# Performance work log

Measured on AMD Instinct MI355X. Metric: run time of the kernel, lower is better.

The kernel has to match this reference:

```python
import jax, jax.numpy as jnp
import numpy as np

N = 100000        # n_nodes (entities)
B = 1024          # batch of users
S = 32            # edge_threshold (sampled edges per node)
M = 64            # adj_matrix neighbors per node
D_IN = 64         # in_channel[0]
HID = 32          # out_channel[0] == in_channel[1]
D_OUT = 64        # out_channel[1]
K_STEP = 2
NUM_SAMPLE = 32
ITEM_LO, ITEM_HI = 0, 39999
SLOPE = 0.01      # leaky_relu default negative slope


def setup_inputs() -> dict:
    key = jax.random.key(0)
    ks = jax.random.split(key, 12)
    sc = lambda *sh: 1.0 / np.sqrt(sh[-1])
    return {
        "entity_embedding": jax.random.normal(ks[0], (N, D_IN), jnp.float32) * 0.1,
        "W1l": jax.random.normal(ks[1], (HID, D_IN), jnp.float32) * sc(HID, D_IN),
        "W1r": jax.random.normal(ks[2], (HID, D_IN), jnp.float32) * sc(HID, D_IN),
        "b1": jnp.zeros((HID,), jnp.float32),
        "W2l": jax.random.normal(ks[3], (D_OUT, HID), jnp.float32) * sc(D_OUT, HID),
        "W2r": jax.random.normal(ks[4], (D_OUT, HID), jnp.float32) * sc(D_OUT, HID),
        "b2": jnp.zeros((D_OUT,), jnp.float32),
        "disc_emb": jax.random.normal(ks[5], (N, D_OUT), jnp.float32) * 0.1,
        "users": jax.random.randint(ks[6], (B,), 0, ITEM_HI + 1, jnp.int32),
        "pos": jax.random.randint(ks[7], (B,), 0, ITEM_HI + 1, jnp.int32),
        "adj_matrix": jax.random.randint(ks[8], (N, M), 0, N, jnp.int32),
        "edge_matrix": jax.random.randint(ks[9], (N, S), 0, N, jnp.int32),
    }


def _leaky(x):
    return jnp.where(x >= 0, x, SLOPE * x)


def _sage(x, src, dst, Wl, Wr, b):
    # PyG SAGEConv: lin_l(mean_{j->i} x_j) + lin_r(x_i)
    sums = jax.ops.segment_sum(x[src], dst, num_segments=N)
    cnt = jax.ops.segment_sum(jnp.ones(src.shape, x.dtype), dst, num_segments=N)
    mean = sums / jnp.maximum(cnt, 1.0)[:, None]
    return mean @ Wl.T + b + x @ Wr.T


def _gcn(x, src, dst, W1l, W1r, b1, W2l, W2r, b2):
    h = _leaky(_sage(x, src, dst, W1l, W1r, b1))   # dropout = identity (eval)
    h = _sage(h, src, dst, W2l, W2r, b2)
    nrm = jnp.sqrt(jnp.sum(h * h, axis=1, keepdims=True))
    return h / jnp.maximum(nrm, 1e-12)             # F.normalize


def _kg_step(gcn, pos_idx, users, adj, explore_flag, step):
    u_e = gcn[users]                               # [B, d]
    pos_e = gcn[pos_idx]                           # [B, d]
    one_hop = adj[pos_idx] if explore_flag == 1 else adj[users]   # [B, M]
    i_e = gcn[one_hop]                             # [B, M, d]
    p = jnp.einsum('bmd,bd->bm', _leaky(pos_e[:, None, :] * i_e), u_e)
    logits = jax.nn.softmax(p, axis=1)
    if step == 1:
        nid = jnp.argmax(logits, axis=1)[:, None]
    else:
        _, nid = jax.lax.top_k(logits, NUM_SAMPLE)
    cand = jnp.take_along_axis(one_hop, nid, axis=1)
    prob = jnp.log(jnp.take_along_axis(logits, nid, axis=1))
    if step == 1:
        return cand[:, 0], prob[:, 0]
    return cand, prob


def _filter_entity(cand, key):
    rnd = jax.random.randint(key, cand.shape, ITEM_LO, ITEM_HI + 1, dtype=cand.dtype)
    bad = (cand > ITEM_HI) | (cand < ITEM_LO)
    return jnp.where(bad, rnd, cand)


def _prune_step(disc_emb, users, pos2, negs, logits):
    # stand-in for discriminator.item_rank (no_grad in original)
    u = jax.lax.stop_gradient(disc_emb[users])
    ranking = jnp.einsum('bd,bjd->bj', u,
                         jax.lax.stop_gradient(disc_emb[pos2] - disc_emb[negs]))
    idx = jnp.argmin(ranking, axis=1)[:, None]
    good_neg = jnp.take_along_axis(negs, idx, axis=1)[:, 0]
    good_logits = jnp.take_along_axis(logits, idx, axis=1)[:, 0]
    return good_neg, good_logits


def reference(entity_embedding, W1l, W1r, b1, W2l, W2r, b2, disc_emb,
              users, pos, adj_matrix, edge_matrix):
    src = jnp.repeat(jnp.arange(N, dtype=jnp.int32), S)   # build_edge node_index
    dst = edge_matrix.reshape(-1)
    gcn = _gcn(entity_embedding, src, dst, W1l, W1r, b1, W2l, W2r, b2)
    fkey = jax.random.key(123)
    neg_list, prob_list = [], []
    p = pos
    for k in range(K_STEP):
        one_hop, one_hop_logits = _kg_step(gcn, p, users, adj_matrix, 1, 1)
        cand, two_logits = _kg_step(gcn, one_hop, users, adj_matrix, 1, 2)
        cand = _filter_entity(cand, jax.random.fold_in(fkey, 2 * k))
        pos2, _ = _kg_step(gcn, p, users, adj_matrix, 2, 2)
        pos2 = _filter_entity(pos2, jax.random.fold_in(fkey, 2 * k + 1))
        good_neg, good_logits = _prune_step(disc_emb, users, pos2, cand, two_logits)
        good_logits = good_logits + one_hop_logits
        neg_list.append(good_neg)
        prob_list.append(good_logits)
        p = good_neg
    return jnp.stack(neg_list), jnp.stack(prob_list)
```

## Files before the change

### kernel.cpp

```cpp
#include <hip/hip_runtime.h>
#include <hip/hip_bf16.h>

#define N_NODES 100000
#define N_EDGES (N_NODES * 32)
#define BATCH   1024
#define SPAN    40000u
#define MULT    7296u
#define FILL_B  (N_EDGES / 256)

#define NB_BKT 391
#define EPB    4096
#define SBLK   782
#define BKT_CAP 8960


__host__ __device__ inline void threefry2x32(unsigned k0, unsigned k1,
                                             unsigned x0, unsigned x1,
                                             unsigned* o0, unsigned* o1)
{
  unsigned ks2 = k0 ^ k1 ^ 0x1BD11BDAu;
  unsigned v0 = x0 + k0, v1 = x1 + k1;
#define RL(x,d) (((x) << (d)) | ((x) >> (32 - (d))))
#define G4(a,b,c,dd) \
  v0 += v1; v1 = RL(v1,a);  v1 ^= v0; \
  v0 += v1; v1 = RL(v1,b);  v1 ^= v0; \
  v0 += v1; v1 = RL(v1,c);  v1 ^= v0; \
  v0 += v1; v1 = RL(v1,dd); v1 ^= v0;
  G4(13,15,26,6)  v0 += k1;  v1 += ks2 + 1u;
  G4(17,29,16,24) v0 += ks2; v1 += k0 + 2u;
  G4(13,15,26,6)  v0 += k0;  v1 += k1 + 3u;
  G4(17,29,16,24) v0 += k1;  v1 += ks2 + 4u;
  G4(13,15,26,6)  v0 += ks2; v1 += k0 + 5u;
#undef G4
#undef RL
  *o0 = v0; *o1 = v1;
}

__device__ __forceinline__ float bcastf(float v, int l)
{
  return __int_as_float(__builtin_amdgcn_readlane(__float_as_int(v), l));
}


__global__ void k_init_buckets(int* __restrict__ bbase, int* __restrict__ bcur)
{
  int i = blockIdx.x * 256 + threadIdx.x;
  if (i < NB_BKT) { bbase[i] = i * BKT_CAP; bcur[i] = i * BKT_CAP; }
}

__global__ __launch_bounds__(256) void k_bucket_hist(
    const int* __restrict__ edge, int* __restrict__ bhist)
{
  __shared__ int h[NB_BKT];
  for (int i = threadIdx.x; i < NB_BKT; i += 256) h[i] = 0;
  __syncthreads();
  int base = blockIdx.x * EPB;
  int cnt = N_EDGES - base; if (cnt > EPB) cnt = EPB;
  const int4* e4 = (const int4*)(edge + base);
  int nq = cnt >> 2;
  for (int i = threadIdx.x; i < nq; i += 256) {
    int4 v = e4[i];
    atomicAdd(&h[v.x >> 8], 1); atomicAdd(&h[v.y >> 8], 1);
    atomicAdd(&h[v.z >> 8], 1); atomicAdd(&h[v.w >> 8], 1);
  }
  __syncthreads();
  for (int i = threadIdx.x; i < NB_BKT; i += 256)
    if (h[i]) atomicAdd(&bhist[i], h[i]);
}

__global__ void k_scan_buckets(const int* __restrict__ bhist,
                               int* __restrict__ bbase, int* __restrict__ bcur)
{
  __shared__ int s[512];
  int t = threadIdx.x;
  s[t] = (t < NB_BKT) ? bhist[t] : 0;
  __syncthreads();
  for (int o = 1; o < 512; o <<= 1) {
    int u = (t >= o) ? s[t - o] : 0;
    __syncthreads();
    s[t] += u;
    __syncthreads();
  }
  if (t < NB_BKT) {
    int excl = s[t] - bhist[t];
    bbase[t] = excl;
    bcur[t]  = excl;
  }
}

__global__ __launch_bounds__(256) void k_bucket_scatter(
    const int* __restrict__ edge, int* __restrict__ bcur,
    int* __restrict__ pairs)
{
  __shared__ int  h[NB_BKT];
  __shared__ int  lbase[NB_BKT];
  __shared__ int  gbase[NB_BKT];
  __shared__ int  lcur[NB_BKT];
  __shared__ int2 buf[EPB];
  int t = threadIdx.x;
  for (int i = t; i < NB_BKT; i += 256) h[i] = 0;
  __syncthreads();
  int base = blockIdx.x * EPB;
  int cnt = N_EDGES - base; if (cnt > EPB) cnt = EPB;
  const int4* e4 = (const int4*)(edge + base);
  int nq = cnt >> 2;
  for (int i = t; i < nq; i += 256) {
    int4 v = e4[i];
    atomicAdd(&h[v.x >> 8], 1); atomicAdd(&h[v.y >> 8], 1);
    atomicAdd(&h[v.z >> 8], 1); atomicAdd(&h[v.w >> 8], 1);
  }
  __syncthreads();
  if (t < 64) {
    int run = 0;
    for (int c = 0; c < NB_BKT; c += 64) {
      int idx = c + t;
      int v = (idx < NB_BKT) ? h[idx] : 0;
      int orig = v;
      for (int o = 1; o < 64; o <<= 1) {
        int u = __shfl_up(v, o);
        if (t >= o) v += u;
      }
      if (idx < NB_BKT) lbase[idx] = run + v - orig;
      run += __shfl(v, 63);
    }
  }
  __syncthreads();
  for (int i = t; i < NB_BKT; i += 256) lcur[i] = lbase[i];
  __syncthreads();
  for (int i = t; i < nq; i += 256) {
    int4 v = e4[i];
    int eid = base + (i << 2);
    int p;
    p = atomicAdd(&lcur[v.x >> 8], 1); buf[p] = make_int2(v.x, (eid + 0) >> 5);
    p = atomicAdd(&lcur[v.y >> 8], 1); buf[p] = make_int2(v.y, (eid + 1) >> 5);
    p = atomicAdd(&lcur[v.z >> 8], 1); buf[p] = make_int2(v.z, (eid + 2) >> 5);
    p = atomicAdd(&lcur[v.w >> 8], 1); buf[p] = make_int2(v.w, (eid + 3) >> 5);
  }
  __syncthreads();
  for (int i = t; i < NB_BKT; i += 256) {
    int c = lcur[i] - lbase[i];
    gbase[i] = (c > 0) ? atomicAdd(&bcur[i], c) : 0;
  }
  __syncthreads();
  for (int i = t; i < cnt; i += 256) {
    int2 pr = buf[i];
    int b = pr.x >> 8;
    pairs[gbase[b] + (i - lbase[b])] = (pr.y << 8) | (pr.x & 255);
  }
}

__global__ __launch_bounds__(256) void k_bucket_csr(
    const int* __restrict__ bbase, const int* __restrict__ bcur,
    const int* __restrict__ pairs, int* __restrict__ csr,
    int* __restrict__ rowp, int* __restrict__ deg)
{
  __shared__ int nd[256], nb[256], nc[256];
  int b = blockIdx.x, t = threadIdx.x;
  int nb0 = b << 8;
  int ebase = bbase[b];
  int ecnt  = bcur[b] - ebase;
  nd[t] = 0; nc[t] = 0;
  __syncthreads();
  for (int i = t; i < ecnt; i += 256) {
    int pr = pairs[ebase + i];
    atomicAdd(&nd[pr & 255], 1);
  }
  __syncthreads();
  nb[t] = nd[t];
  __syncthreads();
  for (int o = 1; o < 256; o <<= 1) {
    int u = (t >= o) ? nb[t - o] : 0;
    __syncthreads();
    nb[t] += u;
    __syncthreads();
  }
  int excl = nb[t] - nd[t];
  int node = nb0 + t;
  if (node < N_NODES) { rowp[node] = ebase + excl; deg[node] = nd[t]; }
  __syncthreads();
  nb[t] = excl;
  __syncthreads();
  for (int i = t; i < ecnt; i += 256) {
    int pr = pairs[ebase + i];
    int l = pr & 255;
    int p = atomicAdd(&nc[l], 1);
    csr[ebase + nb[l] + p] = pr >> 8;
  }
}

__global__ __launch_bounds__(256) void k_gather_csr(
    const int* __restrict__ rowp, const int* __restrict__ deg,
    const int* __restrict__ csr, const float* __restrict__ src,
    float* __restrict__ out)
{
  int node = blockIdx.x * 8 + (threadIdx.x >> 5);
  int f = threadIdx.x & 31;
  int hb = threadIdx.x & 32;
  int sub = f >> 3;
  int q   = f & 7;
  int start = rowp[node];
  int dg = deg[node];
  const float4* src4 = (const float4*)src;
  float4 a0 = make_float4(0.f, 0.f, 0.f, 0.f);
  float4 a1 = make_float4(0.f, 0.f, 0.f, 0.f);
  for (int b0 = 0; b0 < dg; b0 += 32) {
    int idx = b0 + f;
    int e = (idx < dg) ? csr[start + idx] : -1;
#pragma unroll
    for (int j = 0; j < 8; j += 2) {
      int e0 = __shfl(e, hb + 4 * j + sub);
      int e1 = __shfl(e, hb + 4 * (j + 1) + sub);
      if (e0 >= 0) {
        float4 v = src4[(size_t)e0 * 8 + q];
        a0.x += v.x; a0.y += v.y; a0.z += v.z; a0.w += v.w;
      }
      if (e1 >= 0) {
        float4 v = src4[(size_t)e1 * 8 + q];
        a1.x += v.x; a1.y += v.y; a1.z += v.z; a1.w += v.w;
      }
    }
  }
  a0.x += a1.x; a0.y += a1.y; a0.z += a1.z; a0.w += a1.w;
  a0.x += __shfl_xor(a0.x, 8);  a0.y += __shfl_xor(a0.y, 8);
  a0.z += __shfl_xor(a0.z, 8);  a0.w += __shfl_xor(a0.w, 8);
  a0.x += __shfl_xor(a0.x, 16); a0.y += __shfl_xor(a0.y, 16);
  a0.z += __shfl_xor(a0.z, 16); a0.w += __shfl_xor(a0.w, 16);
  if (sub == 0) ((float4*)out)[(size_t)node * 8 + q] = a0;
}

__global__ __launch_bounds__(256) void k_fill_gemm(
    const int* __restrict__ edge, int* __restrict__ head, int* __restrict__ next,
    int nsub, const float* __restrict__ x, const float* __restrict__ W,
    float* __restrict__ y)
{
  __shared__ float sw[32 * 65];
  if (blockIdx.x < FILL_B) {
    int e = blockIdx.x * 256 + threadIdx.x;
    int d = edge[e];
    int sub = e & (nsub - 1);
    int old = atomicExch(head + sub * N_NODES + d, e);
    next[e] = old;
  } else {
    for (int t = threadIdx.x; t < 2048; t += 256) sw[(t >> 6) * 65 + (t & 63)] = W[t];
    __syncthreads();
    int i = (blockIdx.x - FILL_B) * 8 + (threadIdx.x >> 5);
    int f = threadIdx.x & 31;
    const float* xr = x + (size_t)i * 64;
    const float* wr = sw + f * 65;
    float acc = 0.f;
#pragma unroll
    for (int d = 0; d < 64; ++d) acc += xr[d] * wr[d];
    y[(size_t)i * 32 + f] = acc;
  }
}

template<int NSUB>
__global__ __launch_bounds__(256) void k_gather_ll(
    const int* __restrict__ head, const int* __restrict__ next,
    const float* __restrict__ src, float* __restrict__ out,
    int* __restrict__ deg_out)
{
  int node = blockIdx.x * 8 + (threadIdx.x >> 5);
  int f = threadIdx.x & 31;
  int hb = threadIdx.x & 32;
  int e = (f < NSUB) ? head[f * N_NODES + node] : -1;
  float acc = 0.f;
  int cnt = 0;
  while (true) {
    int es[NSUB];
    bool any = false;
#pragma unroll
    for (int j = 0; j < NSUB; ++j) { es[j] = __shfl(e, hb + j); any |= (es[j] != -1); }
    if (!any) break;
    int en = -1;
    if (f < NSUB && e != -1) en = next[e];
#pragma unroll
    for (int j = 0; j < NSUB; ++j)
      if (es[j] != -1) { acc += src[(size_t)(es[j] >> 5) * 32 + f]; cnt++; }
    e = en;
  }
  out[(size_t)node * 32 + f] = acc;
  if (deg_out != nullptr && f == 0) deg_out[node] = cnt;
}

#define DGB 391

__global__ __launch_bounds__(256, 4) void k_gemm64x32(
    const float* __restrict__ x, const float* __restrict__ W, float* __restrict__ y)
{
  int lane = threadIdx.x & 63;
  int wv = blockIdx.x * 4 + (threadIdx.x >> 6);
  int node = wv * 64 + lane;
  bool ok = node < N_NODES;
  const float4* x4 = (const float4*)(x + (size_t)node * 64);
  const float4* W4 = (const float4*)W;
  float acc[32];
#pragma unroll
  for (int o = 0; o < 32; ++o) acc[o] = 0.f;
#pragma unroll 1
  for (int j = 0; j < 16; ++j) {
    float4 xv = ok ? x4[j] : make_float4(0.f, 0.f, 0.f, 0.f);
#pragma unroll
    for (int o = 0; o < 32; ++o) {
      float4 wv4 = W4[o * 16 + j];
      acc[o] += wv4.x * xv.x;
      acc[o] += wv4.y * xv.y;
      acc[o] += wv4.z * xv.z;
      acc[o] += wv4.w * xv.w;
    }
  }
  if (ok) {
    float4* y4 = (float4*)(y + (size_t)node * 32);
#pragma unroll
    for (int k = 0; k < 8; ++k)
      y4[k] = make_float4(acc[4 * k], acc[4 * k + 1], acc[4 * k + 2], acc[4 * k + 3]);
  }
}

__global__ __launch_bounds__(256) void k_scatter(
    const int* __restrict__ edge, const float* __restrict__ src,
    float* __restrict__ acc, int* __restrict__ cnt)
{
  int e = blockIdx.x * 8 + (threadIdx.x >> 5);
  int f = threadIdx.x & 31;
  int d = edge[e];
  atomicAdd(acc + (size_t)d * 32 + f, src[(size_t)(e >> 5) * 32 + f]);
  if (cnt != nullptr && f == 0) atomicAdd(cnt + d, 1);
}

__global__ __launch_bounds__(256, 4) void k_layer1(
    const float* __restrict__ sum1, const int* __restrict__ cnt,
    const float* __restrict__ x, const float* __restrict__ W1r,
    const float* __restrict__ b1, float* __restrict__ h)
{
  int lane = threadIdx.x & 63;
  int wv = blockIdx.x * 4 + (threadIdx.x >> 6);
  int node = wv * 64 + lane;
  bool ok = node < N_NODES;
  const float4* x4 = (const float4*)(x + (size_t)node * 64);
  const float4* W4 = (const float4*)W1r;
  float acc[32];
#pragma unroll
  for (int o = 0; o < 32; ++o) acc[o] = 0.f;
#pragma unroll 1
  for (int j = 0; j < 16; ++j) {
    float4 xv = ok ? x4[j] : make_float4(0.f, 0.f, 0.f, 0.f);
#pragma unroll
    for (int o = 0; o < 32; ++o) {
      float4 wv4 = W4[o * 16 + j];
      acc[o] += wv4.x * xv.x;
      acc[o] += wv4.y * xv.y;
      acc[o] += wv4.z * xv.z;
      acc[o] += wv4.w * xv.w;
    }
  }
  if (ok) {
    float c = fmaxf((float)cnt[node], 1.f);
    const float4* s4 = (const float4*)(sum1 + (size_t)node * 32);
    float4* h4 = (float4*)(h + (size_t)node * 32);
#pragma unroll
    for (int k = 0; k < 8; ++k) {
      float4 sv = s4[k];
      float4 r;
      r.x = ((sv.x / c) + b1[4 * k + 0]) + acc[4 * k + 0];
      r.y = ((sv.y / c) + b1[4 * k + 1]) + acc[4 * k + 1];
      r.z = ((sv.z / c) + b1[4 * k + 2]) + acc[4 * k + 2];
      r.w = ((sv.w / c) + b1[4 * k + 3]) + acc[4 * k + 3];
      r.x = (r.x >= 0.f) ? r.x : 0.01f * r.x;
      r.y = (r.y >= 0.f) ? r.y : 0.01f * r.y;
      r.z = (r.z >= 0.f) ? r.z : 0.01f * r.z;
      r.w = (r.w >= 0.f) ? r.w : 0.01f * r.w;
      h4[k] = r;
    }
  }
}

#define L2_BLOCKS 1250
#define L2_NPW    20
__global__ __launch_bounds__(256) void k_layer2(
    float* __restrict__ A, float* __restrict__ B, const int* __restrict__ cnt,
    const float* __restrict__ W2l, const float* __restrict__ W2r,
    const float* __restrict__ b2)
{
  int lane = threadIdx.x & 63;
  int gw = blockIdx.x * 4 + (threadIdx.x >> 6);
  float wl[32], wr[32];
#pragma unroll
  for (int f = 0; f < 32; ++f) { wl[f] = W2l[lane * 32 + f]; wr[f] = W2r[lane * 32 + f]; }
  float bb = b2[lane];
  int n0 = gw * L2_NPW;
#pragma unroll 1
  for (int i = n0; i < n0 + L2_NPW; ++i) {
    float c = fmaxf((float)cnt[i], 1.f);
    float vin;
    if (lane < 32) vin = B[(size_t)i * 32 + lane] / c;
    else           vin = A[(size_t)i * 32 + (lane - 32)];
    float acc = 0.f, acc2 = 0.f;
#pragma unroll
    for (int f = 0; f < 32; ++f) {
      acc  += bcastf(vin, f)      * wl[f];
      acc2 += bcastf(vin, 32 + f) * wr[f];
    }
    float t = (acc + bb) + acc2;
    float s = t * t;
#pragma unroll
    for (int o = 32; o > 0; o >>= 1) s += __shfl_xor(s, o);
    float g = t / fmaxf(sqrtf(s), 1e-12f);
    if (lane < 32) A[(size_t)i * 32 + lane]        = g;
    else           B[(size_t)i * 32 + (lane - 32)] = g;
  }
}


__device__ inline float kg_score_lds(const float* __restrict__ row,
                                     const float* sp, const float* su)
{
  float acc = 0.f;
#pragma unroll
  for (int d = 0; d < 64; ++d) {
    float t = sp[d] * row[d];
    t = (t >= 0.f) ? t : 0.01f * t;
    acc += t * su[d];
  }
  return acc;
}

__device__ inline float wave_softmax(float acc)
{
  float m = acc;
#pragma unroll
  for (int o = 32; o > 0; o >>= 1) m = fmaxf(m, __shfl_xor(m, o));
  float e = expf(acc - m);
  float Z = e;
#pragma unroll
  for (int o = 32; o > 0; o >>= 1) Z += __shfl_xor(Z, o);
  return e / Z;
}

__device__ inline void load_row(const float* glo, const float* ghi, int node,
                                int lane, float* smem)
{
  smem[lane] = (lane < 32) ? glo[(size_t)node * 32 + lane]
                           : ghi[(size_t)node * 32 + (lane - 32)];
}

__device__ inline void stage_rows(const float* __restrict__ glo,
                                  const float* __restrict__ ghi,
                                  int nb, int lane, float* sn)
{
#pragma unroll
  for (int j = 0; j < 64; ++j) {
    int rj = __builtin_amdgcn_readlane(nb, j);
    float v = (lane < 32) ? glo[(size_t)rj * 32 + lane]
                          : ghi[(size_t)rj * 32 + (lane - 32)];
    sn[j * 65 + lane] = v;
  }
}

__global__ __launch_bounds__(64) void k_kg_argmax(
    const float* __restrict__ glo, const float* __restrict__ ghi,
    const int* __restrict__ users, const int* __restrict__ pvec,
    const int* __restrict__ adj, int* __restrict__ sel_out,
    float* __restrict__ logit_out)
{
  int b = blockIdx.x, lane = threadIdx.x;
  int u = users[b], pb = pvec[b];
  __shared__ float su[64], sp[64];
  __shared__ float sn[64 * 65];
  load_row(glo, ghi, u,  lane, su);
  load_row(glo, ghi, pb, lane, sp);
  int nb = adj[(size_t)pb * 64 + lane];
  stage_rows(glo, ghi, nb, lane, sn);
  __syncthreads();
  float sm = wave_softmax(kg_score_lds(sn + lane * 65, sp, su));
  float v = sm; int i = lane;
#pragma unroll
  for (int o = 32; o > 0; o >>= 1) {
    float ov = __shfl_xor(v, o); int oi = __shfl_xor(i, o);
    if (ov > v || (ov == v && oi < i)) { v = ov; i = oi; }
  }
  float smw = __shfl(sm, i);
  int sel = __shfl(nb, i);
  if (lane == 0) { sel_out[b] = sel; logit_out[b] = logf(smw); }
}

__global__ __launch_bounds__(64) void k_kg_topk2(
    const float* __restrict__ glo, const float* __restrict__ ghi,
    const int* __restrict__ users, const int* __restrict__ srcA,
    const int* __restrict__ pvecB, const int* __restrict__ adj,
    unsigned a1a, unsigned a1b, unsigned a2a, unsigned a2b,
    unsigned c1a, unsigned c1b, unsigned c2a, unsigned c2b,
    int* __restrict__ candA, float* __restrict__ logA, int* __restrict__ candB)
{
  int b = blockIdx.x & (BATCH - 1);
  int var = blockIdx.x >> 10;
  int lane = threadIdx.x;
  int u = users[b];
  int pidx = (var == 0) ? srcA[b] : pvecB[b];
  int nbr  = (var == 0) ? srcA[b] : u;
  unsigned k1a = (var == 0) ? a1a : c1a, k1b = (var == 0) ? a1b : c1b;
  unsigned k2a = (var == 0) ? a2a : c2a, k2b = (var == 0) ? a2b : c2b;
  int* cand_out = (var == 0) ? candA : candB;
  float* logit_out = (var == 0) ? logA : nullptr;

  __shared__ float su[64], sp[64];
  __shared__ float sn[64 * 65];
  load_row(glo, ghi, u,    lane, su);
  load_row(glo, ghi, pidx, lane, sp);
  int nb = adj[(size_t)nbr * 64 + lane];
  stage_rows(glo, ghi, nb, lane, sn);
  __syncthreads();
  float sm = wave_softmax(kg_score_lds(sn + lane * 65, sp, su));
  int r = 0;
#pragma unroll
  for (int j = 0; j < 64; ++j) {
    float sj = bcastf(sm, j);
    if (sj > sm || (sj == sm && j < lane)) ++r;
  }
  if (r < 32) {
    int cand = nb;
    if (logit_out != nullptr) logit_out[b * 32 + r] = logf(sm);
    unsigned j = (unsigned)(b * 32 + r);
    unsigned h0, h1, l0, l1;
    threefry2x32(k1a, k1b, 0u, j, &h0, &h1);
    threefry2x32(k2a, k2b, 0u, j, &l0, &l1);
    unsigned hi = h0 ^ h1, lo = l0 ^ l1;
    unsigned rnd = ((hi % SPAN) * MULT + (lo % SPAN)) % SPAN;
    if (cand > 39999 || cand < 0) cand = (int)rnd;
    cand_out[b * 32 + r] = cand;
  }
}

__global__ __launch_bounds__(64) void k_kg_prune(
    const float* __restrict__ disc, const int* __restrict__ users,
    const int* __restrict__ cand, const float* __restrict__ two_log,
    const int* __restrict__ pos2, const float* __restrict__ one_log,
    float* __restrict__ out, int k, int* __restrict__ p_next)
{
  int b = blockIdx.x, lane = threadIdx.x;
  __shared__ float su[64];
  __shared__ float sd[64 * 65];
  su[lane] = disc[(size_t)users[b] * 64 + lane];
  int pr = (lane < 32) ? pos2[b * 32 + lane] : cand[b * 32 + (lane - 32)];
#pragma unroll
  for (int j = 0; j < 64; ++j) {
    int rj = __builtin_amdgcn_readlane(pr, j);
    sd[j * 65 + lane] = disc[(size_t)rj * 64 + lane];
  }
  __syncthreads();
  float r = 1e30f;
  if (lane < 32) {
    const float* dp = sd + lane * 65;
    const float* dn = sd + (32 + lane) * 65;
    float acc = 0.f;
#pragma unroll
    for (int d = 0; d < 64; ++d) acc += su[d] * (dp[d] - dn[d]);
    r = acc;
  }
  float v = r; int i = lane;
#pragma unroll
  for (int o = 32; o > 0; o >>= 1) {
    float ov = __shfl_xor(v, o); int oi = __shfl_xor(i, o);
    if (ov < v || (ov == v && oi < i)) { v = ov; i = oi; }
  }
  if (lane == 0) {
    int gn = cand[b * 32 + i];
    float gl = two_log[b * 32 + i] + one_log[b];
    out[k * BATCH + b]             = (float)gn;
    out[2 * BATCH + k * BATCH + b] = gl;
    p_next[b] = gn;
  }
}

extern "C" void kernel_launch(void* const* d_in, const int* in_sizes, int n_in,
                              void* d_out, int out_size, void* d_ws, size_t ws_size,
                              hipStream_t stream)
{
  const float* x    = (const float*)d_in[0];
  const float* W1l  = (const float*)d_in[1];
  const float* W1r  = (const float*)d_in[2];
  const float* b1   = (const float*)d_in[3];
  const float* W2l  = (const float*)d_in[4];
  const float* W2r  = (const float*)d_in[5];
  const float* b2   = (const float*)d_in[6];
  const float* disc = (const float*)d_in[7];
  const int*   users= (const int*)d_in[8];
  const int*   pos  = (const int*)d_in[9];
  const int*   adj  = (const int*)d_in[10];
  const int*   edge = (const int*)d_in[11];
  float* out = (float*)d_out;

  char* w = (char*)d_ws;
  const size_t NEED_FIX = 42036480;
  const size_t NEED_CSR = 39617792;
  float *A, *B;
  char* bb;

  if (ws_size >= NEED_FIX) {
    int*  csr   = (int*)(w);
    int*  rowp  = (int*)(w + 14013440);
    int*  deg   = (int*)(w + 14413440);
    int*  bbase = (int*)(w + 14813440);
    int*  bcur  = (int*)(w + 14815488);
    int*  pairs = (int*)(w + 14817536);
    A = (float*)(w + 14817536);
    B = (float*)(w + 28830976);
    bb = w + 41630976;
    k_init_buckets<<<2, 256, 0, stream>>>(bbase, bcur);
    k_bucket_scatter<<<SBLK, 256, 0, stream>>>(edge, bcur, pairs);
    k_bucket_csr<<<NB_BKT, 256, 0, stream>>>(bbase, bcur, pairs, csr, rowp, deg);
    k_gemm64x32<<<DGB, 256, 0, stream>>>(x, W1l, A);
    k_gather_csr<<<N_NODES / 8, 256, 0, stream>>>(rowp, deg, csr, A, B);
    k_layer1<<<DGB, 256, 0, stream>>>(B, deg, x, W1r, b1, A);
    k_gather_csr<<<N_NODES / 8, 256, 0, stream>>>(rowp, deg, csr, A, B);
    k_layer2<<<L2_BLOCKS, 256, 0, stream>>>(A, B, deg, W2l, W2r, b2);
  } else if (ws_size >= NEED_CSR) {
    int*  csr   = (int*)(w);
    int*  rowp  = (int*)(w + 12800000);
    int*  deg   = (int*)(w + 13200000);
    int*  bhist = (int*)(w + 13600000);
    int*  bbase = (int*)(w + 13604096);
    int*  bcur  = (int*)(w + 13608192);
    int*  pairs = (int*)(w + 13612288);
    A = (float*)(w + 13612288);
    B = (float*)(w + 26412288);
    bb = w + 39212288;
    hipMemsetAsync(bhist, 0, 4096, stream);
    k_bucket_hist<<<SBLK, 256, 0, stream>>>(edge, bhist);
    k_scan_buckets<<<1, 512, 0, stream>>>(bhist, bbase, bcur);
    k_bucket_scatter<<<SBLK, 256, 0, stream>>>(edge, bcur, pairs);
    k_bucket_csr<<<NB_BKT, 256, 0, stream>>>(bbase, bcur, pairs, csr, rowp, deg);
    k_gemm64x32<<<DGB, 256, 0, stream>>>(x, W1l, A);
    k_gather_csr<<<N_NODES / 8, 256, 0, stream>>>(rowp, deg, csr, A, B);
    k_layer1<<<DGB, 256, 0, stream>>>(B, deg, x, W1r, b1, A);
    k_gather_csr<<<N_NODES / 8, 256, 0, stream>>>(rowp, deg, csr, A, B);
    k_layer2<<<L2_BLOCKS, 256, 0, stream>>>(A, B, deg, W2l, W2r, b2);
  } else {
    int* cnt = (int*)w;
    A = (float*)(w + 409600);
    B = (float*)(w + 13209600);
    bb = w + 26009600;
    hipMemsetAsync(cnt, 0, 400000, stream);
    hipMemsetAsync(B, 0, 12800000, stream);
    k_gemm64x32<<<DGB, 256, 0, stream>>>(x, W1l, A);
    k_scatter<<<N_EDGES / 8, 256, 0, stream>>>(edge, A, B, cnt);
    k_layer1<<<DGB, 256, 0, stream>>>(B, cnt, x, W1r, b1, A);
    hipMemsetAsync(B, 0, 12800000, stream);
    k_scatter<<<N_EDGES / 8, 256, 0, stream>>>(edge, A, B, nullptr);
    k_layer2<<<L2_BLOCKS, 256, 0, stream>>>(A, B, cnt, W2l, W2r, b2);
  }

  int*   p_cur       = (int*)(bb);
  int*   one_hop_sel = (int*)(bb + 4096);
  float* one_hop_log = (float*)(bb + 8192);
  int*   cand        = (int*)(bb + 12288);
  float* two_log     = (float*)(bb + 143360);
  int*   pos2        = (int*)(bb + 274432);

  for (int k = 0; k < 2; ++k) {
    unsigned f0, f1, a1a, a1b, a2a, a2b, c1a, c1b, c2a, c2b;
    threefry2x32(0u, 123u, 0u, (unsigned)(2 * k), &f0, &f1);
    threefry2x32(f0, f1, 0u, 0u, &a1a, &a1b);
    threefry2x32(f0, f1, 0u, 1u, &a2a, &a2b);
    threefry2x32(0u, 123u, 0u, (unsigned)(2 * k + 1), &f0, &f1);
    threefry2x32(f0, f1, 0u, 0u, &c1a, &c1b);
    threefry2x32(f0, f1, 0u, 1u, &c2a, &c2b);

    const int* pvec = (k == 0) ? pos : p_cur;
    k_kg_argmax<<<BATCH, 64, 0, stream>>>(A, B, users, pvec, adj, one_hop_sel, one_hop_log);
    k_kg_topk2<<<2 * BATCH, 64, 0, stream>>>(A, B, users, one_hop_sel, pvec, adj,
                                             a1a, a1b, a2a, a2b, c1a, c1b, c2a, c2b,
                                             cand, two_log, pos2);
    k_kg_prune<<<BATCH, 64, 0, stream>>>(disc, users, cand, two_log, pos2,
                                         one_hop_log, out, k, p_cur);
  }
}
```

Baseline: 440.8 us.

## Merge bucket scatter and layer-1 GEMM into one heterogeneous launch

Runs the edge bucket-scatter blocks and the x·W1l GEMM blocks in a single kernel launch, selecting the role by block index. Because the GEMM no longer waits for the CSR build, the two independent workloads can overlap on the GPU and one launch is removed. To make this safe, the pairs buffer moves so it no longer aliases A, which the GEMM writes concurrently. It now aliases B instead, which is only written later. The combined kernel needs the scatter's large shared-memory footprint for every block, which can reduce how many GEMM blocks fit on a CU at once.

```diff
diff --git a/kernel.cpp b/kernel.cpp
--- a/kernel.cpp
+++ b/kernel.cpp
@@ -88,19 +88,14 @@
   }
 }
 
-__global__ __launch_bounds__(256) void k_bucket_scatter(
-    const int* __restrict__ edge, int* __restrict__ bcur,
-    int* __restrict__ pairs)
-{
-  __shared__ int  h[NB_BKT];
-  __shared__ int  lbase[NB_BKT];
-  __shared__ int  gbase[NB_BKT];
-  __shared__ int  lcur[NB_BKT];
-  __shared__ int2 buf[EPB];
-  int t = threadIdx.x;
+__device__ __forceinline__ void scatter_body(
+    int bi, int t, const int* __restrict__ edge, int* __restrict__ bcur,
+    int* __restrict__ pairs,
+    int* h, int* lbase, int* gbase, int* lcur, int2* buf)
+{
   for (int i = t; i < NB_BKT; i += 256) h[i] = 0;
   __syncthreads();
-  int base = blockIdx.x * EPB;
+  int base = bi * EPB;
   int cnt = N_EDGES - base; if (cnt > EPB) cnt = EPB;
   const int4* e4 = (const int4*)(edge + base);
   int nq = cnt >> 2;
@@ -146,6 +141,65 @@
     int2 pr = buf[i];
     int b = pr.x >> 8;
     pairs[gbase[b] + (i - lbase[b])] = (pr.y << 8) | (pr.x & 255);
+  }
+}
+
+__global__ __launch_bounds__(256) void k_bucket_scatter(
+    const int* __restrict__ edge, int* __restrict__ bcur,
+    int* __restrict__ pairs)
+{
+  __shared__ int  h[NB_BKT];
+  __shared__ int  lbase[NB_BKT];
+  __shared__ int  gbase[NB_BKT];
+  __shared__ int  lcur[NB_BKT];
+  __shared__ int2 buf[EPB];
+  scatter_body(blockIdx.x, threadIdx.x, edge, bcur, pairs,
+               h, lbase, gbase, lcur, buf);
+}
+
+#define DGB 391
+
+__global__ __launch_bounds__(256, 4) void k_scatter_gemm(
+    const int* __restrict__ edge, int* __restrict__ bcur,
+    int* __restrict__ pairs, const float* __restrict__ x,
+    const float* __restrict__ W, float* __restrict__ y)
+{
+  __shared__ int  h[NB_BKT];
+  __shared__ int  lbase[NB_BKT];
+  __shared__ int  gbase[NB_BKT];
+  __shared__ int  lcur[NB_BKT];
+  __shared__ int2 buf[EPB];
+  if (blockIdx.x < SBLK) {
+    scatter_body(blockIdx.x, threadIdx.x, edge, bcur, pairs,
+                 h, lbase, gbase, lcur, buf);
+  } else {
+    int lane = threadIdx.x & 63;
+    int wv = (blockIdx.x - SBLK) * 4 + (threadIdx.x >> 6);
+    int node = wv * 64 + lane;
+    bool ok = node < N_NODES;
+    const float4* x4 = (const float4*)(x + (size_t)node * 64);
+    const float4* W4 = (const float4*)W;
+    float acc[32];
+#pragma unroll
+    for (int o = 0; o < 32; ++o) acc[o] = 0.f;
+#pragma unroll 1
+    for (int j = 0; j < 16; ++j) {
+      float4 xv = ok ? x4[j] : make_float4(0.f, 0.f, 0.f, 0.f);
+#pragma unroll
+      for (int o = 0; o < 32; ++o) {
+        float4 wv4 = W4[o * 16 + j];
+        acc[o] += wv4.x * xv.x;
+        acc[o] += wv4.y * xv.y;
+        acc[o] += wv4.z * xv.z;
+        acc[o] += wv4.w * xv.w;
+      }
+    }
+    if (ok) {
+      float4* y4 = (float4*)(y + (size_t)node * 32);
+#pragma unroll
+      for (int k = 0; k < 8; ++k)
+        y4[k] = make_float4(acc[4 * k], acc[4 * k + 1], acc[4 * k + 2], acc[4 * k + 3]);
+    }
   }
 }
 
@@ -283,7 +337,6 @@
   if (deg_out != nullptr && f == 0) deg_out[node] = cnt;
 }
 
-#define DGB 391
 
 __global__ __launch_bounds__(256, 4) void k_gemm64x32(
     const float* __restrict__ x, const float* __restrict__ W, float* __restrict__ y)
@@ -602,14 +655,13 @@
     int*  deg   = (int*)(w + 14413440);
     int*  bbase = (int*)(w + 14813440);
     int*  bcur  = (int*)(w + 14815488);
-    int*  pairs = (int*)(w + 14817536);
     A = (float*)(w + 14817536);
-    B = (float*)(w + 28830976);
+    int*  pairs = (int*)(w + 27617536);
+    B = (float*)(w + 27617536);
     bb = w + 41630976;
     k_init_buckets<<<2, 256, 0, stream>>>(bbase, bcur);
-    k_bucket_scatter<<<SBLK, 256, 0, stream>>>(edge, bcur, pairs);
+    k_scatter_gemm<<<SBLK + DGB, 256, 0, stream>>>(edge, bcur, pairs, x, W1l, A);
     k_bucket_csr<<<NB_BKT, 256, 0, stream>>>(bbase, bcur, pairs, csr, rowp, deg);
-    k_gemm64x32<<<DGB, 256, 0, stream>>>(x, W1l, A);
     k_gather_csr<<<N_NODES / 8, 256, 0, stream>>>(rowp, deg, csr, A, B);
     k_layer1<<<DGB, 256, 0, stream>>>(B, deg, x, W1r, b1, A);
     k_gather_csr<<<N_NODES / 8, 256, 0, stream>>>(rowp, deg, csr, A, B);
```

Measured after the change: 434.2 us. No clear change (-1.5%).
